# Optimization experiments

Measured on AMD Instinct MI355X. Metric: run time of the kernel, lower is better.

Reference implementation:

```python
import jax, jax.numpy as jnp
import numpy as np

N_NODES = 100000
N_EDGES = 1600000
D_IN = 256
D_OUT = 128


def setup_inputs() -> dict:
    key = jax.random.key(0)
    k1, k2, k3, k4, k5 = jax.random.split(key, 5)
    x = jax.random.normal(k1, (N_NODES, D_IN), dtype=jnp.float32)
    # Glorot-uniform weight as in weight_variable_glorot
    init_range = np.sqrt(6.0 / (D_IN + D_OUT))
    W = jax.random.uniform(k2, (D_IN, D_OUT), dtype=jnp.float32,
                           minval=-init_range, maxval=init_range)
    adj_rows = jax.random.randint(k3, (N_EDGES,), 0, N_NODES, dtype=jnp.int32)
    adj_cols = jax.random.randint(k4, (N_EDGES,), 0, N_NODES, dtype=jnp.int32)
    adj_vals = jax.random.uniform(k5, (N_EDGES,), dtype=jnp.float32)
    return {"x": x, "W": W, "adj_rows": adj_rows, "adj_cols": adj_cols,
            "adj_vals": adj_vals}


def reference(x, W, adj_rows, adj_cols, adj_vals):
    # dropout with keep_prob = 1 - 0.0 is the identity -> omitted
    h = x @ W                                    # [N, D_OUT] dense projection
    # sparse (COO) adjacency @ h : out[r] += v * h[c]
    msgs = adj_vals[:, None] * h[adj_cols]       # [E, D_OUT]
    agg = jax.ops.segment_sum(msgs, adj_rows, num_segments=N_NODES)
    return jax.nn.relu(agg)                      # act = tf.nn.relu
```

## Files before the change

### kernel.cpp

```cpp
#include <hip/hip_runtime.h>
#include <hip/hip_bf16.h>

#define N_NODES 100000
#define N_EDGES 1600000
#define D_IN 256
#define D_OUT 128
#define CAP 64

typedef short bf16x8 __attribute__((ext_vector_type(8)));
typedef float f32x4 __attribute__((ext_vector_type(4)));
typedef float f32x2 __attribute__((ext_vector_type(2)));

__device__ __forceinline__ unsigned short f2bf(float f) {
    unsigned int u = __builtin_bit_cast(unsigned int, f);
    u += 0x7fffu + ((u >> 16) & 1u);
    return (unsigned short)(u >> 16);
}
__device__ __forceinline__ float bf_lo(unsigned int h) {
    return __builtin_bit_cast(float, h << 16);
}
__device__ __forceinline__ float bf_hi(unsigned int h) {
    return __builtin_bit_cast(float, h & 0xffff0000u);
}

__global__ __launch_bounds__(256) void convert_w(const float* __restrict__ W,
                                                 unsigned short* __restrict__ WbT,
                                                 int* __restrict__ cursor,
                                                 int bucket_mode) {
    int i = blockIdx.x * 256 + threadIdx.x;
    int k = i >> 7;
    int n = i & 127;
    WbT[(size_t)n * D_IN + k] = f2bf(W[i]);
    int z = i * 4;
    if (z < N_NODES) {
        int4 v = bucket_mode ? make_int4(z << 6, (z << 6) + CAP, (z << 6) + 2 * CAP, (z << 6) + 3 * CAP)
                             : make_int4(0, 0, 0, 0);
        *(int4*)(cursor + z) = v;
    }
}

#define GEMM_BLOCKS ((N_NODES + 63) / 64)
#define NWIN 8
#define ROWS_PER_WIN (N_NODES / NWIN)
#define PERM_SLICES 250
__global__ __launch_bounds__(256) void gemm_scatter(const float* __restrict__ x,
                                                    const unsigned short* __restrict__ WbT,
                                                    unsigned short* __restrict__ hb,
                                                    const int* __restrict__ rows,
                                                    const int* __restrict__ cols,
                                                    const float* __restrict__ vals,
                                                    int* __restrict__ cursor,
                                                    int2* __restrict__ buckets) {
    if (blockIdx.x >= GEMM_BLOCKS) {
        const int s     = blockIdx.x - GEMM_BLOCKS;
        const int w     = s & (NWIN - 1);
        const int slice = s >> 3;
        const int lo = w * ROWS_PER_WIN;
        const int hi = lo + ROWS_PER_WIN;
        const int per = (N_EDGES / 4) / PERM_SLICES;
        const int beg = slice * per;
        const int end = beg + per;
        for (int i = beg + (int)threadIdx.x; i < end; i += 256) {
            int4 r = *((const int4*)rows + i);
            const int e = i * 4;
            if (r.x >= lo && r.x < hi) {
                int p = atomicAdd(&cursor[r.x], 1);
                buckets[p] = make_int2(cols[e + 0], __builtin_bit_cast(int, vals[e + 0]));
            }
            if (r.y >= lo && r.y < hi) {
                int p = atomicAdd(&cursor[r.y], 1);
                buckets[p] = make_int2(cols[e + 1], __builtin_bit_cast(int, vals[e + 1]));
            }
            if (r.z >= lo && r.z < hi) {
                int p = atomicAdd(&cursor[r.z], 1);
                buckets[p] = make_int2(cols[e + 2], __builtin_bit_cast(int, vals[e + 2]));
            }
            if (r.w >= lo && r.w < hi) {
                int p = atomicAdd(&cursor[r.w], 1);
                buckets[p] = make_int2(cols[e + 3], __builtin_bit_cast(int, vals[e + 3]));
            }
        }
        return;
    }

    const int wave = threadIdx.x >> 6;
    const int lane = threadIdx.x & 63;
    const int row0 = blockIdx.x * 64 + wave * 16;
    if (row0 >= N_NODES) return;
    const int m = lane & 15;
    const int q = lane >> 4;

    const float* xr = x + (size_t)(row0 + m) * D_IN + q * 8;

    float4 a[8][2];
#pragma unroll
    for (int kc = 0; kc < 8; ++kc) {
        a[kc][0] = *(const float4*)(xr + kc * 32);
        a[kc][1] = *(const float4*)(xr + kc * 32 + 4);
    }

    bf16x8 af[8];
#pragma unroll
    for (int kc = 0; kc < 8; ++kc) {
        af[kc][0] = (short)f2bf(a[kc][0].x); af[kc][1] = (short)f2bf(a[kc][0].y);
        af[kc][2] = (short)f2bf(a[kc][0].z); af[kc][3] = (short)f2bf(a[kc][0].w);
        af[kc][4] = (short)f2bf(a[kc][1].x); af[kc][5] = (short)f2bf(a[kc][1].y);
        af[kc][6] = (short)f2bf(a[kc][1].z); af[kc][7] = (short)f2bf(a[kc][1].w);
    }

    f32x4 acc[8];
#pragma unroll
    for (int nt = 0; nt < 8; ++nt) acc[nt] = (f32x4){0.f, 0.f, 0.f, 0.f};

#pragma unroll
    for (int kc = 0; kc < 8; ++kc) {
        const int kb = kc * 32 + q * 8;
#pragma unroll
        for (int nt = 0; nt < 8; ++nt) {
            bf16x8 bf = *(const bf16x8*)(WbT + (size_t)(nt * 16 + m) * D_IN + kb);
            acc[nt] = __builtin_amdgcn_mfma_f32_16x16x32_bf16(af[kc], bf, acc[nt], 0, 0, 0);
        }
    }

#pragma unroll
    for (int nt = 0; nt < 8; ++nt)
#pragma unroll
        for (int r = 0; r < 4; ++r) {
            int grow = row0 + q * 4 + r;
            hb[(size_t)grow * D_OUT + nt * 16 + m] = f2bf(acc[nt][r]);
        }
}

__global__ __launch_bounds__(256) void gather_bucket(const int* __restrict__ cursor,
                                                     const int2* __restrict__ buckets,
                                                     const unsigned short* __restrict__ hb,
                                                     float* __restrict__ out) {
    int row  = blockIdx.x * 4 + (threadIdx.x >> 6);
    int lane = threadIdx.x & 63;
    if (row >= N_NODES) return;
    int beg = row << 6;
    int end = __builtin_amdgcn_readfirstlane(cursor[row]);

    float ax0 = 0.f, ay0 = 0.f, ax1 = 0.f, ay1 = 0.f;
    float ax2 = 0.f, ay2 = 0.f, ax3 = 0.f, ay3 = 0.f;
    int j = beg;
    for (; j + 4 <= end; j += 4) {
        int4 p01 = *(const int4*)(buckets + j);
        int4 p23 = *(const int4*)(buckets + j + 2);
        unsigned int h0 = *(const unsigned int*)(hb + (size_t)p01.x * D_OUT + lane * 2);
        unsigned int h1 = *(const unsigned int*)(hb + (size_t)p01.z * D_OUT + lane * 2);
        unsigned int h2 = *(const unsigned int*)(hb + (size_t)p23.x * D_OUT + lane * 2);
        unsigned int h3 = *(const unsigned int*)(hb + (size_t)p23.z * D_OUT + lane * 2);
        float v0 = __builtin_bit_cast(float, p01.y);
        float v1 = __builtin_bit_cast(float, p01.w);
        float v2 = __builtin_bit_cast(float, p23.y);
        float v3 = __builtin_bit_cast(float, p23.w);
        ax0 = fmaf(v0, bf_lo(h0), ax0); ay0 = fmaf(v0, bf_hi(h0), ay0);
        ax1 = fmaf(v1, bf_lo(h1), ax1); ay1 = fmaf(v1, bf_hi(h1), ay1);
        ax2 = fmaf(v2, bf_lo(h2), ax2); ay2 = fmaf(v2, bf_hi(h2), ay2);
        ax3 = fmaf(v3, bf_lo(h3), ax3); ay3 = fmaf(v3, bf_hi(h3), ay3);
    }
    for (; j < end; ++j) {
        int2 e = buckets[j];
        unsigned int h = *(const unsigned int*)(hb + (size_t)e.x * D_OUT + lane * 2);
        float v = __builtin_bit_cast(float, e.y);
        ax0 = fmaf(v, bf_lo(h), ax0);
        ay0 = fmaf(v, bf_hi(h), ay0);
    }
    float accx = (ax0 + ax1) + (ax2 + ax3);
    float accy = (ay0 + ay1) + (ay2 + ay3);
    f32x2 o;
    o[0] = fmaxf(accx, 0.f);
    o[1] = fmaxf(accy, 0.f);
    __builtin_nontemporal_store(o, (f32x2*)(out + (size_t)row * D_OUT + lane * 2));
}

__global__ __launch_bounds__(256) void gemm_mfma(const float* __restrict__ x,
                                                 const unsigned short* __restrict__ WbT,
                                                 unsigned short* __restrict__ hb) {
    const int wave = threadIdx.x >> 6;
    const int lane = threadIdx.x & 63;
    const int row0 = blockIdx.x * 64 + wave * 16;
    if (row0 >= N_NODES) return;
    const int m = lane & 15;
    const int q = lane >> 4;

    const float* xr = x + (size_t)(row0 + m) * D_IN + q * 8;

    float4 a[8][2];
#pragma unroll
    for (int kc = 0; kc < 8; ++kc) {
        a[kc][0] = *(const float4*)(xr + kc * 32);
        a[kc][1] = *(const float4*)(xr + kc * 32 + 4);
    }

    bf16x8 af[8];
#pragma unroll
    for (int kc = 0; kc < 8; ++kc) {
        af[kc][0] = (short)f2bf(a[kc][0].x); af[kc][1] = (short)f2bf(a[kc][0].y);
        af[kc][2] = (short)f2bf(a[kc][0].z); af[kc][3] = (short)f2bf(a[kc][0].w);
        af[kc][4] = (short)f2bf(a[kc][1].x); af[kc][5] = (short)f2bf(a[kc][1].y);
        af[kc][6] = (short)f2bf(a[kc][1].z); af[kc][7] = (short)f2bf(a[kc][1].w);
    }

    f32x4 acc[8];
#pragma unroll
    for (int nt = 0; nt < 8; ++nt) acc[nt] = (f32x4){0.f, 0.f, 0.f, 0.f};

#pragma unroll
    for (int kc = 0; kc < 8; ++kc) {
        const int kb = kc * 32 + q * 8;
#pragma unroll
        for (int nt = 0; nt < 8; ++nt) {
            bf16x8 bf = *(const bf16x8*)(WbT + (size_t)(nt * 16 + m) * D_IN + kb);
            acc[nt] = __builtin_amdgcn_mfma_f32_16x16x32_bf16(af[kc], bf, acc[nt], 0, 0, 0);
        }
    }

#pragma unroll
    for (int nt = 0; nt < 8; ++nt)
#pragma unroll
        for (int r = 0; r < 4; ++r) {
            int grow = row0 + q * 4 + r;
            hb[(size_t)grow * D_OUT + nt * 16 + m] = f2bf(acc[nt][r]);
        }
}

__global__ __launch_bounds__(256) void hist_rows(const int* __restrict__ rows,
                                                 int* __restrict__ counts) {
    int i = blockIdx.x * 256 + threadIdx.x;
    if (i < N_EDGES / 4) {
        int4 r = *(const int4*)(rows + i * 4);
        atomicAdd(&counts[r.x], 1);
        atomicAdd(&counts[r.y], 1);
        atomicAdd(&counts[r.z], 1);
        atomicAdd(&counts[r.w], 1);
    }
}

#define SCHUNK 1024
#define NSCAN ((N_NODES + SCHUNK - 1) / SCHUNK)
__global__ __launch_bounds__(1024) void scan_reduce(const int* __restrict__ counts,
                                                    int* __restrict__ bsum, int n) {
    __shared__ int ws[16];
    const int t = threadIdx.x, lane = t & 63, wid = t >> 6;
    int i = blockIdx.x * SCHUNK + t;
    int v = (i < n) ? counts[i] : 0;
#pragma unroll
    for (int off = 32; off >= 1; off >>= 1) v += __shfl_down(v, off);
    if (lane == 0) ws[wid] = v;
    __syncthreads();
    if (t == 0) {
        int s = 0;
#pragma unroll
        for (int w = 0; w < 16; ++w) s += ws[w];
        bsum[blockIdx.x] = s;
    }
}

__global__ __launch_bounds__(1024) void scan_apply(const int* __restrict__ counts,
                                                   const int* __restrict__ bsum,
                                                   int* __restrict__ ptr,
                                                   int* __restrict__ cursor, int n, int nb) {
    __shared__ int wtot[16];
    __shared__ int bpre[128];
    const int t = threadIdx.x, lane = t & 63, wid = t >> 6;
    int i = blockIdx.x * SCHUNK + t;
    int v = (i < n) ? counts[i] : 0;
    int x = v;
#pragma unroll
    for (int off = 1; off < 64; off <<= 1) {
        int u = __shfl_up(x, off);
        if (lane >= off) x += u;
    }
    if (lane == 63) wtot[wid] = x;

    if (wid == 0) {
        int carry = 0;
        for (int base = 0; base < nb; base += 64) {
            int idx = base + lane;
            int bv = (idx < nb) ? bsum[idx] : 0;
            int bx = bv;
#pragma unroll
            for (int off = 1; off < 64; off <<= 1) {
                int u = __shfl_up(bx, off);
                if (lane >= off) bx += u;
            }
            if (idx < nb) bpre[idx] = bx - bv + carry;
            carry += __shfl(bx, 63);
        }
    }
    __syncthreads();
    if (wid == 0) {
        int wv = (lane < 16) ? wtot[lane] : 0;
        int y = wv;
#pragma unroll
        for (int off = 1; off < 16; off <<= 1) {
            int u = __shfl_up(y, off);
            if (lane >= off) y += u;
        }
        if (lane < 16) wtot[lane] = y - wv;
    }
    __syncthreads();
    int excl = (x - v) + wtot[wid] + bpre[blockIdx.x];
    if (i < n) {
        ptr[i] = excl;
        cursor[i] = excl;
        if (i == n - 1) ptr[n] = excl + v;
    }
}

__global__ __launch_bounds__(256) void permute_edges(const int* __restrict__ rows,
                                                     const int* __restrict__ cols,
                                                     const float* __restrict__ vals,
                                                     int* __restrict__ cursor,
                                                     int2* __restrict__ edge_r) {
    const int w     = blockIdx.x & 7;
    const int slice = blockIdx.x >> 3;
    const int lo = w * (N_NODES / 8);
    const int hi = lo + (N_NODES / 8);
    const int per = (N_EDGES / 4) / PERM_SLICES;
    const int beg = slice * per;
    const int end = beg + per;
    for (int i = beg + (int)threadIdx.x; i < end; i += 256) {
        int4 r = *((const int4*)rows + i);
        const int e = i * 4;
        if (r.x >= lo && r.x < hi) {
            int p = atomicAdd(&cursor[r.x], 1);
            edge_r[p] = make_int2(cols[e + 0], __builtin_bit_cast(int, vals[e + 0]));
        }
        if (r.y >= lo && r.y < hi) {
            int p = atomicAdd(&cursor[r.y], 1);
            edge_r[p] = make_int2(cols[e + 1], __builtin_bit_cast(int, vals[e + 1]));
        }
        if (r.z >= lo && r.z < hi) {
            int p = atomicAdd(&cursor[r.z], 1);
            edge_r[p] = make_int2(cols[e + 2], __builtin_bit_cast(int, vals[e + 2]));
        }
        if (r.w >= lo && r.w < hi) {
            int p = atomicAdd(&cursor[r.w], 1);
            edge_r[p] = make_int2(cols[e + 3], __builtin_bit_cast(int, vals[e + 3]));
        }
    }
}

__global__ __launch_bounds__(256) void gather_rows(const int* __restrict__ ptr,
                                                   const int2* __restrict__ edge_r,
                                                   const unsigned short* __restrict__ hb,
                                                   float* __restrict__ out) {
    int row  = blockIdx.x * 4 + (threadIdx.x >> 6);
    int lane = threadIdx.x & 63;
    if (row >= N_NODES) return;
    int beg = __builtin_amdgcn_readfirstlane(ptr[row]);
    int end = __builtin_amdgcn_readfirstlane(ptr[row + 1]);

    float ax0 = 0.f, ay0 = 0.f, ax1 = 0.f, ay1 = 0.f;
    float ax2 = 0.f, ay2 = 0.f, ax3 = 0.f, ay3 = 0.f;
    int j = beg;
    for (; j + 4 <= end; j += 4) {
        int2 e0 = edge_r[j + 0];
        int2 e1 = edge_r[j + 1];
        int2 e2 = edge_r[j + 2];
        int2 e3 = edge_r[j + 3];
        unsigned int h0 = *(const unsigned int*)(hb + (size_t)e0.x * D_OUT + lane * 2);
        unsigned int h1 = *(const unsigned int*)(hb + (size_t)e1.x * D_OUT + lane * 2);
        unsigned int h2 = *(const unsigned int*)(hb + (size_t)e2.x * D_OUT + lane * 2);
        unsigned int h3 = *(const unsigned int*)(hb + (size_t)e3.x * D_OUT + lane * 2);
        float v0 = __builtin_bit_cast(float, e0.y);
        float v1 = __builtin_bit_cast(float, e1.y);
        float v2 = __builtin_bit_cast(float, e2.y);
        float v3 = __builtin_bit_cast(float, e3.y);
        ax0 = fmaf(v0, bf_lo(h0), ax0); ay0 = fmaf(v0, bf_hi(h0), ay0);
        ax1 = fmaf(v1, bf_lo(h1), ax1); ay1 = fmaf(v1, bf_hi(h1), ay1);
        ax2 = fmaf(v2, bf_lo(h2), ax2); ay2 = fmaf(v2, bf_hi(h2), ay2);
        ax3 = fmaf(v3, bf_lo(h3), ax3); ay3 = fmaf(v3, bf_hi(h3), ay3);
    }
    for (; j < end; ++j) {
        int2 e = edge_r[j];
        unsigned int h = *(const unsigned int*)(hb + (size_t)e.x * D_OUT + lane * 2);
        float v = __builtin_bit_cast(float, e.y);
        ax0 = fmaf(v, bf_lo(h), ax0);
        ay0 = fmaf(v, bf_hi(h), ay0);
    }
    float accx = (ax0 + ax1) + (ax2 + ax3);
    float accy = (ay0 + ay1) + (ay2 + ay3);
    float2 o = make_float2(fmaxf(accx, 0.f), fmaxf(accy, 0.f));
    *(float2*)(out + (size_t)row * D_OUT + lane * 2) = o;
}

extern "C" void kernel_launch(void* const* d_in, const int* in_sizes, int n_in,
                              void* d_out, int out_size, void* d_ws, size_t ws_size,
                              hipStream_t stream) {
    const float* x    = (const float*)d_in[0];
    const float* W    = (const float*)d_in[1];
    const int*   rows = (const int*)d_in[2];
    const int*   cols = (const int*)d_in[3];
    const float* vals = (const float*)d_in[4];
    float* out = (float*)d_out;

    char* ws = (char*)d_ws;
    size_t off = 0;
    unsigned short* hb  = (unsigned short*)(ws + off); off += ((size_t)N_NODES * D_OUT * 2 + 255) & ~(size_t)255;
    unsigned short* WbT = (unsigned short*)(ws + off); off += ((size_t)D_IN * D_OUT * 2 + 255) & ~(size_t)255;
    int*  cursor = (int*)(ws + off); off += ((size_t)N_NODES * 4 + 255) & ~(size_t)255;

    const size_t bucket_bytes = (size_t)N_NODES * CAP * 8;

    if (ws_size >= off + bucket_bytes) {
        int2* buckets = (int2*)(ws + off);
        convert_w<<<(D_IN * D_OUT) / 256, 256, 0, stream>>>(W, WbT, cursor, 1);
        gemm_scatter<<<GEMM_BLOCKS + NWIN * PERM_SLICES, 256, 0, stream>>>(
            x, WbT, hb, rows, cols, vals, cursor, buckets);
        gather_bucket<<<(N_NODES + 3) / 4, 256, 0, stream>>>(cursor, buckets, hb, out);
    } else {
        int*  ptr    = (int*)(ws + off); size_t off2 = off + (((size_t)(N_NODES + 1) * 4 + 255) & ~(size_t)255);
        int2* edge_r = (int2*)(ws + off2); off2 += ((size_t)N_EDGES * 8 + 255) & ~(size_t)255;
        int*  bsum   = (int*)(ws + off2);

        convert_w<<<(D_IN * D_OUT) / 256, 256, 0, stream>>>(W, WbT, cursor, 0);
        gemm_mfma<<<GEMM_BLOCKS, 256, 0, stream>>>(x, WbT, hb);
        hist_rows<<<(N_EDGES / 4 + 255) / 256, 256, 0, stream>>>(rows, cursor);
        scan_reduce<<<NSCAN, 1024, 0, stream>>>(cursor, bsum, N_NODES);
        scan_apply<<<NSCAN, 1024, 0, stream>>>(cursor, bsum, ptr, cursor, N_NODES, NSCAN);
        permute_edges<<<NWIN * PERM_SLICES, 256, 0, stream>>>(rows, cols, vals, cursor, edge_r);
        gather_rows<<<(N_NODES + 3) / 4, 256, 0, stream>>>(ptr, edge_r, hb, out);
    }
}
```

Baseline: 375.0 us.

## Interleave GEMM and scatter blocks, widen GEMM tile, unroll gather by eight

The fused kernel now interleaves its work: of every seven consecutive blocks, two run the projection GEMM and five run the edge scatter. Before, all GEMM blocks came first and all scatter blocks after, so the compute-heavy and atomic-heavy work can now share the GPU at the same time. Each GEMM wave now covers 32 rows instead of 16, so every loaded W fragment is reused across two MFMAs, and the x loads are spread across the k loop instead of being staged up front. The gather loop adds an 8-edge unrolled body with eight independent accumulators to keep more loads in flight. The cost is higher register pressure in both kernels and a grid whose block-to-work mapping is hard-coded.

```diff
diff --git a/kernel.cpp b/kernel.cpp
--- a/kernel.cpp
+++ b/kernel.cpp
@@ -39,10 +39,11 @@
     }
 }
 
-#define GEMM_BLOCKS ((N_NODES + 63) / 64)
+#define GEMM_UNITS 782
 #define NWIN 8
 #define ROWS_PER_WIN (N_NODES / NWIN)
 #define PERM_SLICES 250
+#define FUSED_GRID 2800
 __global__ __launch_bounds__(256) void gemm_scatter(const float* __restrict__ x,
                                                     const unsigned short* __restrict__ WbT,
                                                     unsigned short* __restrict__ hb,
@@ -51,8 +52,11 @@
                                                     const float* __restrict__ vals,
                                                     int* __restrict__ cursor,
                                                     int2* __restrict__ buckets) {
-    if (blockIdx.x >= GEMM_BLOCKS) {
-        const int s     = blockIdx.x - GEMM_BLOCKS;
+    const int b = blockIdx.x;
+    const int phase = b % 7;
+    if (phase >= 2) {
+        const int s = (b / 7) * 5 + (phase - 2);
+        if (s >= NWIN * PERM_SLICES) return;
         const int w     = s & (NWIN - 1);
         const int slice = s >> 3;
         const int lo = w * ROWS_PER_WIN;
@@ -83,52 +87,57 @@
         return;
     }
 
+    const int g = (b / 7) * 2 + phase;
+    if (g >= GEMM_UNITS) return;
     const int wave = threadIdx.x >> 6;
     const int lane = threadIdx.x & 63;
-    const int row0 = blockIdx.x * 64 + wave * 16;
+    const int row0 = g * 128 + wave * 32;
     if (row0 >= N_NODES) return;
     const int m = lane & 15;
     const int q = lane >> 4;
 
-    const float* xr = x + (size_t)(row0 + m) * D_IN + q * 8;
-
-    float4 a[8][2];
-#pragma unroll
-    for (int kc = 0; kc < 8; ++kc) {
-        a[kc][0] = *(const float4*)(xr + kc * 32);
-        a[kc][1] = *(const float4*)(xr + kc * 32 + 4);
-    }
-
-    bf16x8 af[8];
-#pragma unroll
-    for (int kc = 0; kc < 8; ++kc) {
-        af[kc][0] = (short)f2bf(a[kc][0].x); af[kc][1] = (short)f2bf(a[kc][0].y);
-        af[kc][2] = (short)f2bf(a[kc][0].z); af[kc][3] = (short)f2bf(a[kc][0].w);
-        af[kc][4] = (short)f2bf(a[kc][1].x); af[kc][5] = (short)f2bf(a[kc][1].y);
-        af[kc][6] = (short)f2bf(a[kc][1].z); af[kc][7] = (short)f2bf(a[kc][1].w);
-    }
-
-    f32x4 acc[8];
-#pragma unroll
-    for (int nt = 0; nt < 8; ++nt) acc[nt] = (f32x4){0.f, 0.f, 0.f, 0.f};
+    const float* xr0 = x + (size_t)(row0 + m) * D_IN;
+    const float* xr1 = x + (size_t)(row0 + 16 + m) * D_IN;
+
+    f32x4 acc[2][8];
+#pragma unroll
+    for (int h = 0; h < 2; ++h)
+#pragma unroll
+        for (int nt = 0; nt < 8; ++nt) acc[h][nt] = (f32x4){0.f, 0.f, 0.f, 0.f};
 
 #pragma unroll
     for (int kc = 0; kc < 8; ++kc) {
         const int kb = kc * 32 + q * 8;
+        float4 a00 = *(const float4*)(xr0 + kb);
+        float4 a01 = *(const float4*)(xr0 + kb + 4);
+        float4 a10 = *(const float4*)(xr1 + kb);
+        float4 a11 = *(const float4*)(xr1 + kb + 4);
+        bf16x8 af0, af1;
+        af0[0] = (short)f2bf(a00.x); af0[1] = (short)f2bf(a00.y);
+        af0[2] = (short)f2bf(a00.z); af0[3] = (short)f2bf(a00.w);
+        af0[4] = (short)f2bf(a01.x); af0[5] = (short)f2bf(a01.y);
+        af0[6] = (short)f2bf(a01.z); af0[7] = (short)f2bf(a01.w);
+        af1[0] = (short)f2bf(a10.x); af1[1] = (short)f2bf(a10.y);
+        af1[2] = (short)f2bf(a10.z); af1[3] = (short)f2bf(a10.w);
+        af1[4] = (short)f2bf(a11.x); af1[5] = (short)f2bf(a11.y);
+        af1[6] = (short)f2bf(a11.z); af1[7] = (short)f2bf(a11.w);
 #pragma unroll
         for (int nt = 0; nt < 8; ++nt) {
             bf16x8 bf = *(const bf16x8*)(WbT + (size_t)(nt * 16 + m) * D_IN + kb);
-            acc[nt] = __builtin_amdgcn_mfma_f32_16x16x32_bf16(af[kc], bf, acc[nt], 0, 0, 0);
-        }
-    }
-
-#pragma unroll
-    for (int nt = 0; nt < 8; ++nt)
-#pragma unroll
-        for (int r = 0; r < 4; ++r) {
-            int grow = row0 + q * 4 + r;
-            hb[(size_t)grow * D_OUT + nt * 16 + m] = f2bf(acc[nt][r]);
-        }
+            acc[0][nt] = __builtin_amdgcn_mfma_f32_16x16x32_bf16(af0, bf, acc[0][nt], 0, 0, 0);
+            acc[1][nt] = __builtin_amdgcn_mfma_f32_16x16x32_bf16(af1, bf, acc[1][nt], 0, 0, 0);
+        }
+    }
+
+#pragma unroll
+    for (int h = 0; h < 2; ++h)
+#pragma unroll
+        for (int nt = 0; nt < 8; ++nt)
+#pragma unroll
+            for (int r = 0; r < 4; ++r) {
+                int grow = row0 + h * 16 + q * 4 + r;
+                hb[(size_t)grow * D_OUT + nt * 16 + m] = f2bf(acc[h][nt][r]);
+            }
 }
 
 __global__ __launch_bounds__(256) void gather_bucket(const int* __restrict__ cursor,
@@ -143,7 +152,39 @@
 
     float ax0 = 0.f, ay0 = 0.f, ax1 = 0.f, ay1 = 0.f;
     float ax2 = 0.f, ay2 = 0.f, ax3 = 0.f, ay3 = 0.f;
+    float ax4 = 0.f, ay4 = 0.f, ax5 = 0.f, ay5 = 0.f;
+    float ax6 = 0.f, ay6 = 0.f, ax7 = 0.f, ay7 = 0.f;
     int j = beg;
+    for (; j + 8 <= end; j += 8) {
+        int4 p01 = *(const int4*)(buckets + j);
+        int4 p23 = *(const int4*)(buckets + j + 2);
+        int4 p45 = *(const int4*)(buckets + j + 4);
+        int4 p67 = *(const int4*)(buckets + j + 6);
+        unsigned int h0 = *(const unsigned int*)(hb + (size_t)p01.x * D_OUT + lane * 2);
+        unsigned int h1 = *(const unsigned int*)(hb + (size_t)p01.z * D_OUT + lane * 2);
+        unsigned int h2 = *(const unsigned int*)(hb + (size_t)p23.x * D_OUT + lane * 2);
+        unsigned int h3 = *(const unsigned int*)(hb + (size_t)p23.z * D_OUT + lane * 2);
+        unsigned int h4 = *(const unsigned int*)(hb + (size_t)p45.x * D_OUT + lane * 2);
+        unsigned int h5 = *(const unsigned int*)(hb + (size_t)p45.z * D_OUT + lane * 2);
+        unsigned int h6 = *(const unsigned int*)(hb + (size_t)p67.x * D_OUT + lane * 2);
+        unsigned int h7 = *(const unsigned int*)(hb + (size_t)p67.z * D_OUT + lane * 2);
+        float v0 = __builtin_bit_cast(float, p01.y);
+        float v1 = __builtin_bit_cast(float, p01.w);
+        float v2 = __builtin_bit_cast(float, p23.y);
+        float v3 = __builtin_bit_cast(float, p23.w);
+        float v4 = __builtin_bit_cast(float, p45.y);
+        float v5 = __builtin_bit_cast(float, p45.w);
+        float v6 = __builtin_bit_cast(float, p67.y);
+        float v7 = __builtin_bit_cast(float, p67.w);
+        ax0 = fmaf(v0, bf_lo(h0), ax0); ay0 = fmaf(v0, bf_hi(h0), ay0);
+        ax1 = fmaf(v1, bf_lo(h1), ax1); ay1 = fmaf(v1, bf_hi(h1), ay1);
+        ax2 = fmaf(v2, bf_lo(h2), ax2); ay2 = fmaf(v2, bf_hi(h2), ay2);
+        ax3 = fmaf(v3, bf_lo(h3), ax3); ay3 = fmaf(v3, bf_hi(h3), ay3);
+        ax4 = fmaf(v4, bf_lo(h4), ax4); ay4 = fmaf(v4, bf_hi(h4), ay4);
+        ax5 = fmaf(v5, bf_lo(h5), ax5); ay5 = fmaf(v5, bf_hi(h5), ay5);
+        ax6 = fmaf(v6, bf_lo(h6), ax6); ay6 = fmaf(v6, bf_hi(h6), ay6);
+        ax7 = fmaf(v7, bf_lo(h7), ax7); ay7 = fmaf(v7, bf_hi(h7), ay7);
+    }
     for (; j + 4 <= end; j += 4) {
         int4 p01 = *(const int4*)(buckets + j);
         int4 p23 = *(const int4*)(buckets + j + 2);
@@ -167,8 +208,8 @@
         ax0 = fmaf(v, bf_lo(h), ax0);
         ay0 = fmaf(v, bf_hi(h), ay0);
     }
-    float accx = (ax0 + ax1) + (ax2 + ax3);
-    float accy = (ay0 + ay1) + (ay2 + ay3);
+    float accx = ((ax0 + ax1) + (ax2 + ax3)) + ((ax4 + ax5) + (ax6 + ax7));
+    float accy = ((ay0 + ay1) + (ay2 + ay3)) + ((ay4 + ay5) + (ay6 + ay7));
     f32x2 o;
     o[0] = fmaxf(accx, 0.f);
     o[1] = fmaxf(accy, 0.f);
@@ -409,7 +450,7 @@
     if (ws_size >= off + bucket_bytes) {
         int2* buckets = (int2*)(ws + off);
         convert_w<<<(D_IN * D_OUT) / 256, 256, 0, stream>>>(W, WbT, cursor, 1);
-        gemm_scatter<<<GEMM_BLOCKS + NWIN * PERM_SLICES, 256, 0, stream>>>(
+        gemm_scatter<<<FUSED_GRID, 256, 0, stream>>>(
             x, WbT, hb, rows, cols, vals, cursor, buckets);
         gather_bucket<<<(N_NODES + 3) / 4, 256, 0, stream>>>(cursor, buckets, hb, out);
     } else {
@@ -418,7 +459,7 @@
         int*  bsum   = (int*)(ws + off2);
 
         convert_w<<<(D_IN * D_OUT) / 256, 256, 0, stream>>>(W, WbT, cursor, 0);
-        gemm_mfma<<<GEMM_BLOCKS, 256, 0, stream>>>(x, WbT, hb);
+        gemm_mfma<<<(N_NODES + 63) / 64, 256, 0, stream>>>(x, WbT, hb);
         hist_rows<<<(N_EDGES / 4 + 255) / 256, 256, 0, stream>>>(rows, cursor);
         scan_reduce<<<NSCAN, 1024, 0, stream>>>(cursor, bsum, N_NODES);
         scan_apply<<<NSCAN, 1024, 0, stream>>>(cursor, bsum, ptr, cursor, N_NODES, NSCAN);
```

After: 373.2 us. About the same (-0.5%).
